# Kernel optimization log

Hardware: AMD Instinct MI355X
Metric: run time of the kernel (lower is better)

The kernel has to match this reference:

```python
import jax, jax.numpy as jnp
import numpy as np

B, S, V, H = 512, 2048, 29, 128  # batch, seq_len, vocab(input_size), hidden_size


def setup_inputs() -> dict:
    key = jax.random.key(0)
    ks = jax.random.split(key, 9)
    ke = 1.0 / np.sqrt(H)  # torch nn.RNN init bound for encoder
    kd = 1.0 / np.sqrt(V)  # decoder hidden_size = V
    u = lambda k, shape, b: jax.random.uniform(k, shape, jnp.float32, -b, b)
    return {
        "x": jax.random.normal(ks[0], (B, S, V), jnp.float32),
        "We_ih": u(ks[1], (H, V), ke),
        "We_hh": u(ks[2], (H, H), ke),
        "be_ih": u(ks[3], (H,), ke),
        "be_hh": u(ks[4], (H,), ke),
        "Wd_ih": u(ks[5], (V, H), kd),
        "Wd_hh": u(ks[6], (V, V), kd),
        "bd_ih": u(ks[7], (V,), kd),
        "bd_hh": u(ks[8], (V,), kd),
    }


def reference(x, We_ih, We_hh, be_ih, be_hh, Wd_ih, Wd_hh, bd_ih, bd_hh):
    b, s, _ = x.shape
    # ---- encoder: vanilla tanh RNN over sequence, keep final hidden state ----
    # precompute input projections for all steps: (S, B, H)
    xp = jnp.einsum("bsv,hv->sbh", x, We_ih) + be_ih + be_hh
    def enc_step(h, xt):
        h = jnp.tanh(xt + h @ We_hh.T)
        return h, None
    h0 = jnp.zeros((b, We_hh.shape[0]), x.dtype)
    encoded, _ = jax.lax.scan(enc_step, h0, xp)  # (B, H)
    # ---- decoder: feeds the same `encoded` vector at every step ----
    dec_in = encoded @ Wd_ih.T + bd_ih + bd_hh  # (B, V), constant across steps
    def dec_step(h, _):
        h = jnp.tanh(dec_in + h @ Wd_hh.T)
        return h, h
    hd0 = jnp.zeros((b, Wd_hh.shape[0]), x.dtype)
    _, outs = jax.lax.scan(dec_step, hd0, None, length=s)  # (S, B, V)
    return jnp.transpose(outs, (1, 0, 2))  # (B, S, V)
```

## Files before the change

### kernel.cpp

```cpp
#include <hip/hip_runtime.h>
#include <hip/hip_bf16.h>

#define BB 512
#define SS 2048
#define VV 29
#define HH 128

__device__ __forceinline__ float fast_tanh(float z) {
    float az = fabsf(z);
    float e  = __expf(-2.0f * az);
    float r  = 1.0f - 2.0f * e * __builtin_amdgcn_rcpf(1.0f + e);
    return copysignf(r, z);
}

__global__ __launch_bounds__(256) void rnn_fused(
    const float* __restrict__ x,
    const float* __restrict__ We_ih,
    const float* __restrict__ We_hh,
    const float* __restrict__ be_ih,
    const float* __restrict__ be_hh,
    const float* __restrict__ Wd_ih,
    const float* __restrict__ Wd_hh,
    const float* __restrict__ bd_ih,
    const float* __restrict__ bd_hh,
    float* __restrict__ out)
{
    const int b   = blockIdx.x;
    const int tid = threadIdx.x;
    const int wv  = tid >> 6;
    const int l   = tid & 63;
    const int i   = (wv << 5) + (l >> 1);
    const int g   = l & 1;

    __shared__ float hbuf[2][HH];
    __shared__ float xbuf[2][32];

    float w[64];
    const float* wrow = We_hh + i * HH + g * 64;
    #pragma unroll
    for (int j = 0; j < 64; ++j) w[j] = wrow[j];

    const int xv0 = g ? 15 : 0;
    const int xn  = g ? 14 : 15;
    float wx[15];
    #pragma unroll
    for (int j = 0; j < 15; ++j) wx[j] = (j < xn) ? We_ih[i * VV + xv0 + j] : 0.0f;

    const float bias = (g == 0) ? (be_ih[i] + be_hh[i]) : 0.0f;

    const float* xb = x + (size_t)b * SS * VV;

    if (tid < HH) hbuf[0][tid] = 0.0f;
    if (tid < 32) {
        xbuf[0][tid] = (tid < VV) ? xb[tid] : 0.0f;
        xbuf[1][tid] = 0.0f;
    }
    __syncthreads();

#define ENC_STEP(CUR, NXT, T)                                              \
    {                                                                      \
        float xpre = 0.0f;                                                 \
        {                                                                  \
            int tn = (T) + 1; if (tn >= SS) tn = SS - 1;                   \
            if (wv == 0 && l < VV) xpre = xb[tn * VV + l];                 \
        }                                                                  \
        float a0 = 0.f, a1 = 0.f, a2 = 0.f, a3 = 0.f;                      \
        const float* hb = &hbuf[CUR][g * 64];                              \
        _Pragma("unroll")                                                  \
        for (int j = 0; j < 64; j += 4) {                                  \
            a0 += w[j + 0] * hb[j + 0];                                    \
            a1 += w[j + 1] * hb[j + 1];                                    \
            a2 += w[j + 2] * hb[j + 2];                                    \
            a3 += w[j + 3] * hb[j + 3];                                    \
        }                                                                  \
        float accx = bias;                                                 \
        _Pragma("unroll")                                                  \
        for (int j = 0; j < 15; ++j) accx += wx[j] * xbuf[CUR][xv0 + j];   \
        float p = (a0 + a1) + (a2 + a3) + accx;                            \
        float q = __shfl_xor(p, 1, 64);                                    \
        float hn = fast_tanh(p + q);     \
        hbuf[NXT][i] = hn;             \
        if (wv == 0 && l < VV) xbuf[NXT][l] = xpre;                        \
        __syncthreads();                                                   \
    }

    for (int t = 0; t < SS; t += 2) {
        ENC_STEP(0, 1, t)
        ENC_STEP(1, 0, t + 1)
    }

    if (tid >= 64) return;
    const int lane = tid;
    const int r = (lane < VV) ? lane : (VV - 1);

    float di = bd_ih[r] + bd_hh[r];
    {
        const float* wdi = Wd_ih + r * HH;
        float d0 = 0.f, d1 = 0.f, d2 = 0.f, d3 = 0.f;
        #pragma unroll
        for (int j = 0; j < HH; j += 4) {
            d0 += wdi[j + 0] * hbuf[0][j + 0];
            d1 += wdi[j + 1] * hbuf[0][j + 1];
            d2 += wdi[j + 2] * hbuf[0][j + 2];
            d3 += wdi[j + 3] * hbuf[0][j + 3];
        }
        di += (d0 + d1) + (d2 + d3);
    }

    float wd[VV];
    {
        const float* wdr = Wd_hh + r * VV;
        #pragma unroll
        for (int j = 0; j < VV; ++j) wd[j] = wdr[j];
    }

    float hd = 0.0f;
    float* ob = out + (size_t)b * SS * VV;
    int t = 0;
    for (; t < SS; ++t) {
        float a0 = di, a1 = 0.f, a2 = 0.f, a3 = 0.f;
        #pragma unroll
        for (int j = 0; j < VV; j += 4) {
            a0 += wd[j] * __shfl(hd, j, 64);
            if (j + 1 < VV) a1 += wd[j + 1] * __shfl(hd, j + 1, 64);
            if (j + 2 < VV) a2 += wd[j + 2] * __shfl(hd, j + 2, 64);
            if (j + 3 < VV) a3 += wd[j + 3] * __shfl(hd, j + 3, 64);
        }
        float hn = fast_tanh((a0 + a1) + (a2 + a3));
        int conv = (fabsf(hn - hd) < 1e-6f) ? 1 : 0;
        hd = hn;
        if (lane < VV) ob[(size_t)t * VV + lane] = hn;
        if (__all(conv)) { ++t; break; }
    }

    if (t < SS) {
        while (t & 3) {
            if (lane < VV) ob[(size_t)t * VV + lane] = hd;
            ++t;
        }
        if (t < SS) {
            const int phi = (4 * lane) % VV;
            float4 v4;
            v4.x = __shfl(hd, phi, 64);
            v4.y = __shfl(hd, (phi + 1) % VV, 64);
            v4.z = __shfl(hd, (phi + 2) % VV, 64);
            v4.w = __shfl(hd, (phi + 3) % VV, 64);
            if (lane < 58) {
                const long fend = (long)SS * VV;
                for (long f = (long)t * VV + 4 * lane; f + 4 <= fend; f += 232) {
                    *reinterpret_cast<float4*>(ob + f) = v4;
                }
            }
        }
    }
}

extern "C" void kernel_launch(void* const* d_in, const int* in_sizes, int n_in,
                              void* d_out, int out_size, void* d_ws, size_t ws_size,
                              hipStream_t stream) {
    const float* x     = (const float*)d_in[0];
    const float* We_ih = (const float*)d_in[1];
    const float* We_hh = (const float*)d_in[2];
    const float* be_ih = (const float*)d_in[3];
    const float* be_hh = (const float*)d_in[4];
    const float* Wd_ih = (const float*)d_in[5];
    const float* Wd_hh = (const float*)d_in[6];
    const float* bd_ih = (const float*)d_in[7];
    const float* bd_hh = (const float*)d_in[8];
    float* out = (float*)d_out;

    rnn_fused<<<dim3(BB), dim3(256), 0, stream>>>(
        x, We_ih, We_hh, be_ih, be_hh, Wd_ih, Wd_hh, bd_ih, bd_hh, out);
}
```

Before: 1.671 ms.

## Assign one encoder hidden unit per thread with 128-thread blocks and deeper x prefetch

Each thread now owns a full row of We_hh (128 registers) instead of splitting it across two lanes. This drops the per-step shuffle reduction and halves the block to 128 threads (2 waves). Hidden state and inputs are read from shared memory as float4 vectors, and x is prefetched two steps ahead through rotating registers to hide global load latency. The trade-off is higher register pressure and twice the serial FMA work per thread, in exchange for fewer waves per barrier and less LDS traffic.

```diff
diff --git a/kernel.cpp b/kernel.cpp
--- a/kernel.cpp
+++ b/kernel.cpp
@@ -13,7 +13,7 @@
     return copysignf(r, z);
 }
 
-__global__ __launch_bounds__(256) void rnn_fused(
+__global__ __launch_bounds__(128, 1) void rnn_fused(
     const float* __restrict__ x,
     const float* __restrict__ We_ih,
     const float* __restrict__ We_hh,
@@ -27,66 +27,77 @@
 {
     const int b   = blockIdx.x;
     const int tid = threadIdx.x;
-    const int wv  = tid >> 6;
-    const int l   = tid & 63;
-    const int i   = (wv << 5) + (l >> 1);
-    const int g   = l & 1;
+    const int i   = tid;
 
     __shared__ float hbuf[2][HH];
     __shared__ float xbuf[2][32];
 
-    float w[64];
-    const float* wrow = We_hh + i * HH + g * 64;
+    float wh[HH];
+    {
+        const float4* wrow4 = reinterpret_cast<const float4*>(We_hh + (size_t)i * HH);
+        #pragma unroll
+        for (int j = 0; j < HH / 4; ++j) {
+            float4 v = wrow4[j];
+            wh[4 * j + 0] = v.x; wh[4 * j + 1] = v.y;
+            wh[4 * j + 2] = v.z; wh[4 * j + 3] = v.w;
+        }
+    }
+    float wx[32];
     #pragma unroll
-    for (int j = 0; j < 64; ++j) w[j] = wrow[j];
-
-    const int xv0 = g ? 15 : 0;
-    const int xn  = g ? 14 : 15;
-    float wx[15];
-    #pragma unroll
-    for (int j = 0; j < 15; ++j) wx[j] = (j < xn) ? We_ih[i * VV + xv0 + j] : 0.0f;
-
-    const float bias = (g == 0) ? (be_ih[i] + be_hh[i]) : 0.0f;
+    for (int j = 0; j < 32; ++j) wx[j] = (j < VV) ? We_ih[i * VV + j] : 0.0f;
+    const float bias = be_ih[i] + be_hh[i];
 
     const float* xb = x + (size_t)b * SS * VV;
 
-    if (tid < HH) hbuf[0][tid] = 0.0f;
+    hbuf[0][tid] = 0.0f;
     if (tid < 32) {
         xbuf[0][tid] = (tid < VV) ? xb[tid] : 0.0f;
         xbuf[1][tid] = 0.0f;
     }
+
+    float xA = 0.0f, xB = 0.0f;
+    if (tid < VV) {
+        xA = xb[VV + tid];
+        xB = xb[2 * VV + tid];
+    }
     __syncthreads();
 
-#define ENC_STEP(CUR, NXT, T)                                              \
+#define ENC_STEP(CUR, NXT, T, XREG)                                        \
     {                                                                      \
-        float xpre = 0.0f;                                                 \
+        float xnew = 0.0f;                                                 \
         {                                                                  \
-            int tn = (T) + 1; if (tn >= SS) tn = SS - 1;                   \
-            if (wv == 0 && l < VV) xpre = xb[tn * VV + l];                 \
+            int tn = (T) + 3; if (tn >= SS) tn = SS - 1;                   \
+            if (tid < VV) xnew = xb[tn * VV + tid];                        \
         }                                                                  \
-        float a0 = 0.f, a1 = 0.f, a2 = 0.f, a3 = 0.f;                      \
-        const float* hb = &hbuf[CUR][g * 64];                              \
+        float a0 = bias, a1 = 0.f, a2 = 0.f, a3 = 0.f;                     \
+        const float4* hb4 = reinterpret_cast<const float4*>(&hbuf[CUR][0]);\
         _Pragma("unroll")                                                  \
-        for (int j = 0; j < 64; j += 4) {                                  \
-            a0 += w[j + 0] * hb[j + 0];                                    \
-            a1 += w[j + 1] * hb[j + 1];                                    \
-            a2 += w[j + 2] * hb[j + 2];                                    \
-            a3 += w[j + 3] * hb[j + 3];                                    \
+        for (int j = 0; j < HH / 4; ++j) {                                 \
+            float4 hv = hb4[j];                                            \
+            a0 += wh[4 * j + 0] * hv.x;                                    \
+            a1 += wh[4 * j + 1] * hv.y;                                    \
+            a2 += wh[4 * j + 2] * hv.z;                                    \
+            a3 += wh[4 * j + 3] * hv.w;                                    \
         }                                                                  \
-        float accx = bias;                                                 \
+        const float4* xb4 = reinterpret_cast<const float4*>(&xbuf[CUR][0]);\
         _Pragma("unroll")                                                  \
-        for (int j = 0; j < 15; ++j) accx += wx[j] * xbuf[CUR][xv0 + j];   \
-        float p = (a0 + a1) + (a2 + a3) + accx;                            \
-        float q = __shfl_xor(p, 1, 64);                                    \
-        float hn = fast_tanh(p + q);     \
-        hbuf[NXT][i] = hn;             \
-        if (wv == 0 && l < VV) xbuf[NXT][l] = xpre;                        \
+        for (int k = 0; k < 8; ++k) {                                      \
+            float4 xv = xb4[k];                                            \
+            a0 += wx[4 * k + 0] * xv.x;                                    \
+            a1 += wx[4 * k + 1] * xv.y;                                    \
+            a2 += wx[4 * k + 2] * xv.z;                                    \
+            a3 += wx[4 * k + 3] * xv.w;                                    \
+        }                                                                  \
+        float hn = fast_tanh((a0 + a1) + (a2 + a3));                       \
+        hbuf[NXT][i] = hn;                                                 \
+        if (tid < VV) xbuf[NXT][tid] = XREG;   \
+        XREG = xnew;                               \
         __syncthreads();                                                   \
     }
 
     for (int t = 0; t < SS; t += 2) {
-        ENC_STEP(0, 1, t)
-        ENC_STEP(1, 0, t + 1)
+        ENC_STEP(0, 1, t,     xA)
+        ENC_STEP(1, 0, t + 1, xB)
     }
 
     if (tid >= 64) return;
@@ -169,6 +180,6 @@
     const float* bd_hh = (const float*)d_in[8];
     float* out = (float*)d_out;
 
-    rnn_fused<<<dim3(BB), dim3(256), 0, stream>>>(
+    rnn_fused<<<dim3(BB), dim3(128), 0, stream>>>(
         x, We_ih, We_hh, be_ih, be_hh, Wd_ih, Wd_hh, bd_ih, bd_hh, out);
 }
```

Measured after the change: 2.376 ms. 1.42x slower.

## Batch 16 sequences per block and run encoder recurrence on bf16x3 MFMA

Applied to the files above, without the earlier changes.

Each block now handles 16 batch rows instead of one. The encoder's hidden-state matvec becomes a small matrix multiply on MFMA bf16 instructions. Weights, hidden state and inputs are split into hi/lo bf16 pairs, and three products are summed to keep near-fp32 accuracy. Input x is loaded in 16-step chunks that are double-buffered and converted in shared memory, and the decoder runs two passes of half-wave groups per wave. This amortizes per-step barrier and latency cost across many sequences, but the launch shrinks to 32 blocks, and the split-bf16 products may lose precision relative to fp32.

```diff
diff --git a/kernel.cpp b/kernel.cpp
--- a/kernel.cpp
+++ b/kernel.cpp
@@ -5,6 +5,12 @@
 #define SS 2048
 #define VV 29
 #define HH 128
+#define NC 16
+#define NBLK (BB / NC)
+#define CH 16
+
+typedef __attribute__((ext_vector_type(8))) short bf16x8;
+typedef __attribute__((ext_vector_type(4))) float f32x4;
 
 __device__ __forceinline__ float fast_tanh(float z) {
     float az = fabsf(z);
@@ -12,8 +18,22 @@
     float r  = 1.0f - 2.0f * e * __builtin_amdgcn_rcpf(1.0f + e);
     return copysignf(r, z);
 }
-
-__global__ __launch_bounds__(256) void rnn_fused(
+__device__ __forceinline__ unsigned bf16_rne(float f) {
+    unsigned u = __float_as_uint(f);
+    return (u + 0x7fffu + ((u >> 16) & 1u)) >> 16;
+}
+__device__ __forceinline__ float bfbits2f(unsigned b) { return __uint_as_float(b << 16); }
+__device__ __forceinline__ bf16x8 as_bf16x8(uint4 v) { union { uint4 q; bf16x8 s; } u; u.q = v; return u.s; }
+
+#define MF(A, B, C) __builtin_amdgcn_mfma_f32_16x16x32_bf16((A), (B), (C), 0, 0, 0)
+
+#define BLOCK_SYNC do {                                        \
+    asm volatile("s_waitcnt lgkmcnt(0)" ::: "memory");         \
+    __builtin_amdgcn_s_barrier();                              \
+    asm volatile("" ::: "memory");                             \
+} while (0)
+
+__global__ __launch_bounds__(256, 1) void rnn_fused(
     const float* __restrict__ x,
     const float* __restrict__ We_ih,
     const float* __restrict__ We_hh,
@@ -25,130 +45,272 @@
     const float* __restrict__ bd_hh,
     float* __restrict__ out)
 {
-    const int b   = blockIdx.x;
     const int tid = threadIdx.x;
-    const int wv  = tid >> 6;
+    const int w   = tid >> 6;
     const int l   = tid & 63;
-    const int i   = (wv << 5) + (l >> 1);
-    const int g   = l & 1;
-
-    __shared__ float hbuf[2][HH];
-    __shared__ float xbuf[2][32];
-
-    float w[64];
-    const float* wrow = We_hh + i * HH + g * 64;
+    const int c   = l & 15;
+    const int g   = l >> 4;
+    const int b0  = blockIdx.x * NC;
+
+    __shared__ uint4 shHhi[2][4][4][16];
+    __shared__ uint4 shHlo[2][4][4][16];
+    __shared__ uint4 shXhi[2][CH][4][17];
+    __shared__ uint4 shXlo[2][CH][4][17];
+    __shared__ float hdec[NC][HH];
+
+    bf16x8 whiA[4], wloA[4], whiB[4], wloB[4];
+    bf16x8 wxhiA, wxloA, wxhiB, wxloB;
+    {
+        const int m0 = 16 * (2 * w)     + c;
+        const int m1 = 16 * (2 * w + 1) + c;
+        const float* r0 = We_hh + (size_t)m0 * HH;
+        const float* r1 = We_hh + (size_t)m1 * HH;
+        #pragma unroll
+        for (int kt = 0; kt < 4; ++kt) {
+            union { unsigned u[4]; bf16x8 s; } HA, LA, HB, LB;
+            #pragma unroll
+            for (int p = 0; p < 4; ++p) {
+                int e0 = 32 * kt + 8 * g + 2 * p;
+                float fa0 = r0[e0], fa1 = r0[e0 + 1];
+                float fb0 = r1[e0], fb1 = r1[e0 + 1];
+                unsigned ha0 = bf16_rne(fa0), ha1 = bf16_rne(fa1);
+                unsigned hb0 = bf16_rne(fb0), hb1 = bf16_rne(fb1);
+                HA.u[p] = ha0 | (ha1 << 16);
+                HB.u[p] = hb0 | (hb1 << 16);
+                LA.u[p] = bf16_rne(fa0 - bfbits2f(ha0)) | (bf16_rne(fa1 - bfbits2f(ha1)) << 16);
+                LB.u[p] = bf16_rne(fb0 - bfbits2f(hb0)) | (bf16_rne(fb1 - bfbits2f(hb1)) << 16);
+            }
+            whiA[kt] = HA.s; wloA[kt] = LA.s;
+            whiB[kt] = HB.s; wloB[kt] = LB.s;
+        }
+        const float* q0 = We_ih + (size_t)m0 * VV;
+        const float* q1 = We_ih + (size_t)m1 * VV;
+        union { unsigned u[4]; bf16x8 s; } HA, LA, HB, LB;
+        #pragma unroll
+        for (int p = 0; p < 4; ++p) {
+            int k0 = 8 * g + 2 * p;
+            float fa0 = (k0     < VV) ? q0[k0]     : 0.f;
+            float fa1 = (k0 + 1 < VV) ? q0[k0 + 1] : 0.f;
+            float fb0 = (k0     < VV) ? q1[k0]     : 0.f;
+            float fb1 = (k0 + 1 < VV) ? q1[k0 + 1] : 0.f;
+            unsigned ha0 = bf16_rne(fa0), ha1 = bf16_rne(fa1);
+            unsigned hb0 = bf16_rne(fb0), hb1 = bf16_rne(fb1);
+            HA.u[p] = ha0 | (ha1 << 16);
+            HB.u[p] = hb0 | (hb1 << 16);
+            LA.u[p] = bf16_rne(fa0 - bfbits2f(ha0)) | (bf16_rne(fa1 - bfbits2f(ha1)) << 16);
+            LB.u[p] = bf16_rne(fb0 - bfbits2f(hb0)) | (bf16_rne(fb1 - bfbits2f(hb1)) << 16);
+        }
+        wxhiA = HA.s; wxloA = LA.s; wxhiB = HB.s; wxloB = LB.s;
+    }
+
+    f32x4 bias0v, bias1v;
     #pragma unroll
-    for (int j = 0; j < 64; ++j) w[j] = wrow[j];
-
-    const int xv0 = g ? 15 : 0;
-    const int xn  = g ? 14 : 15;
-    float wx[15];
-    #pragma unroll
-    for (int j = 0; j < 15; ++j) wx[j] = (j < xn) ? We_ih[i * VV + xv0 + j] : 0.0f;
-
-    const float bias = (g == 0) ? (be_ih[i] + be_hh[i]) : 0.0f;
-
-    const float* xb = x + (size_t)b * SS * VV;
-
-    if (tid < HH) hbuf[0][tid] = 0.0f;
-    if (tid < 32) {
-        xbuf[0][tid] = (tid < VV) ? xb[tid] : 0.0f;
-        xbuf[1][tid] = 0.0f;
-    }
+    for (int q = 0; q < 4; ++q) {
+        int ra = 16 * (2 * w)     + 4 * g + q;
+        int rb = 16 * (2 * w + 1) + 4 * g + q;
+        bias0v[q] = be_ih[ra] + be_hh[ra];
+        bias1v[q] = be_ih[rb] + be_hh[rb];
+    }
+
+    const int c0 = tid >> 4;
+    const int t0 = tid & 15;
+    const float* xrowc = x + (size_t)(b0 + c0) * SS * VV;
+    float xv[VV];
+
+#define XLOAD(CHUNK) {                                                          \
+        const float* p_ = xrowc + (size_t)((CHUNK) * CH + t0) * VV;             \
+        _Pragma("unroll")                                                       \
+        for (int j = 0; j < VV; ++j) xv[j] = p_[j]; }
+
+#define XCONVERT(CB) {                                                          \
+        unsigned hb[VV + 1], lb[VV + 1];                                        \
+        _Pragma("unroll")                                                       \
+        for (int j = 0; j < VV; ++j) {                                          \
+            unsigned h_ = bf16_rne(xv[j]);                                      \
+            hb[j] = h_; lb[j] = bf16_rne(xv[j] - bfbits2f(h_));                 \
+        }                                                                       \
+        hb[VV] = 0u; lb[VV] = 0u;                                               \
+        _Pragma("unroll")                                                       \
+        for (int m = 0; m < 15; ++m) {                                          \
+            int g_ = m >> 2, w_ = m & 3;                                        \
+            ((unsigned*)&shXhi[CB][t0][g_][c0])[w_] = hb[2*m] | (hb[2*m+1] << 16); \
+            ((unsigned*)&shXlo[CB][t0][g_][c0])[w_] = lb[2*m] | (lb[2*m+1] << 16); \
+        }                                                                       \
+        ((unsigned*)&shXhi[CB][t0][3][c0])[3] = 0u;            \
+        ((unsigned*)&shXlo[CB][t0][3][c0])[3] = 0u; }
+
+    {
+        uint4 z = make_uint4(0u, 0u, 0u, 0u);
+        ((uint4*)shHhi)[tid] = z; ((uint4*)shHhi)[tid + 256] = z;
+        ((uint4*)shHlo)[tid] = z; ((uint4*)shHlo)[tid + 256] = z;
+    }
+    XLOAD(0);
     __syncthreads();
-
-#define ENC_STEP(CUR, NXT, T)                                              \
-    {                                                                      \
-        float xpre = 0.0f;                                                 \
-        {                                                                  \
-            int tn = (T) + 1; if (tn >= SS) tn = SS - 1;                   \
-            if (wv == 0 && l < VV) xpre = xb[tn * VV + l];                 \
-        }                                                                  \
-        float a0 = 0.f, a1 = 0.f, a2 = 0.f, a3 = 0.f;                      \
-        const float* hb = &hbuf[CUR][g * 64];                              \
-        _Pragma("unroll")                                                  \
-        for (int j = 0; j < 64; j += 4) {                                  \
-            a0 += w[j + 0] * hb[j + 0];                                    \
-            a1 += w[j + 1] * hb[j + 1];                                    \
-            a2 += w[j + 2] * hb[j + 2];                                    \
-            a3 += w[j + 3] * hb[j + 3];                                    \
-        }                                                                  \
-        float accx = bias;                                                 \
-        _Pragma("unroll")                                                  \
-        for (int j = 0; j < 15; ++j) accx += wx[j] * xbuf[CUR][xv0 + j];   \
-        float p = (a0 + a1) + (a2 + a3) + accx;                            \
-        float q = __shfl_xor(p, 1, 64);                                    \
-        float hn = fast_tanh(p + q);     \
-        hbuf[NXT][i] = hn;             \
-        if (wv == 0 && l < VV) xbuf[NXT][l] = xpre;                        \
-        __syncthreads();                                                   \
-    }
-
-    for (int t = 0; t < SS; t += 2) {
-        ENC_STEP(0, 1, t)
-        ENC_STEP(1, 0, t + 1)
-    }
-
-    if (tid >= 64) return;
-    const int lane = tid;
-    const int r = (lane < VV) ? lane : (VV - 1);
-
-    float di = bd_ih[r] + bd_hh[r];
+    XCONVERT(0);
+    XLOAD(1);
+    BLOCK_SYNC;
+
+#define ENC_STEP(CUR, NXT, SLOC, CB)                                            \
+    {                                                                           \
+        bf16x8 Bh0 = as_bf16x8(shHhi[CUR][0][g][c]);                            \
+        bf16x8 Bh1 = as_bf16x8(shHhi[CUR][1][g][c]);                            \
+        bf16x8 Bh2 = as_bf16x8(shHhi[CUR][2][g][c]);                            \
+        bf16x8 Bh3 = as_bf16x8(shHhi[CUR][3][g][c]);                            \
+        bf16x8 Bl0 = as_bf16x8(shHlo[CUR][0][g][c]);                            \
+        bf16x8 Bl1 = as_bf16x8(shHlo[CUR][1][g][c]);                            \
+        bf16x8 Bl2 = as_bf16x8(shHlo[CUR][2][g][c]);                            \
+        bf16x8 Bl3 = as_bf16x8(shHlo[CUR][3][g][c]);                            \
+        bf16x8 Bx  = as_bf16x8(shXhi[CB][SLOC][g][c]);                          \
+        bf16x8 Bxl = as_bf16x8(shXlo[CB][SLOC][g][c]);                          \
+        f32x4 d0a = bias0v, d1a = bias1v;                                       \
+        f32x4 d0b = {0.f,0.f,0.f,0.f}, d1b = {0.f,0.f,0.f,0.f};                 \
+        f32x4 d0c = {0.f,0.f,0.f,0.f}, d1c = {0.f,0.f,0.f,0.f};                 \
+        d0a = MF(whiA[0], Bh0, d0a);  d1a = MF(whiB[0], Bh0, d1a);              \
+        d0b = MF(wloA[0], Bh0, d0b);  d1b = MF(wloB[0], Bh0, d1b);              \
+        d0c = MF(whiA[0], Bl0, d0c);  d1c = MF(whiB[0], Bl0, d1c);              \
+        d0a = MF(whiA[1], Bh1, d0a);  d1a = MF(whiB[1], Bh1, d1a);              \
+        d0b = MF(wloA[1], Bh1, d0b);  d1b = MF(wloB[1], Bh1, d1b);              \
+        d0c = MF(whiA[1], Bl1, d0c);  d1c = MF(whiB[1], Bl1, d1c);              \
+        d0a = MF(whiA[2], Bh2, d0a);  d1a = MF(whiB[2], Bh2, d1a);              \
+        d0b = MF(wloA[2], Bh2, d0b);  d1b = MF(wloB[2], Bh2, d1b);              \
+        d0c = MF(whiA[2], Bl2, d0c);  d1c = MF(whiB[2], Bl2, d1c);              \
+        d0a = MF(whiA[3], Bh3, d0a);  d1a = MF(whiB[3], Bh3, d1a);              \
+        d0b = MF(wloA[3], Bh3, d0b);  d1b = MF(wloB[3], Bh3, d1b);              \
+        d0c = MF(whiA[3], Bl3, d0c);  d1c = MF(whiB[3], Bl3, d1c);              \
+        d0a = MF(wxhiA, Bx, d0a);     d1a = MF(wxhiB, Bx, d1a);                 \
+        d0b = MF(wxloA, Bx, d0b);     d1b = MF(wxloB, Bx, d1b);                 \
+        d0c = MF(wxhiA, Bxl, d0c);    d1c = MF(wxhiB, Bxl, d1c);                \
+        float hn00 = fast_tanh(d0a[0] + d0b[0] + d0c[0]);                       \
+        float hn01 = fast_tanh(d0a[1] + d0b[1] + d0c[1]);                       \
+        float hn02 = fast_tanh(d0a[2] + d0b[2] + d0c[2]);                       \
+        float hn03 = fast_tanh(d0a[3] + d0b[3] + d0c[3]);                       \
+        float hn10 = fast_tanh(d1a[0] + d1b[0] + d1c[0]);                       \
+        float hn11 = fast_tanh(d1a[1] + d1b[1] + d1c[1]);                       \
+        float hn12 = fast_tanh(d1a[2] + d1b[2] + d1c[2]);                       \
+        float hn13 = fast_tanh(d1a[3] + d1b[3] + d1c[3]);                       \
+        unsigned h00 = bf16_rne(hn00), h01 = bf16_rne(hn01);                    \
+        unsigned h02 = bf16_rne(hn02), h03 = bf16_rne(hn03);                    \
+        unsigned h10 = bf16_rne(hn10), h11 = bf16_rne(hn11);                    \
+        unsigned h12 = bf16_rne(hn12), h13 = bf16_rne(hn13);                    \
+        unsigned l00 = bf16_rne(hn00 - bfbits2f(h00));                          \
+        unsigned l01 = bf16_rne(hn01 - bfbits2f(h01));                          \
+        unsigned l02 = bf16_rne(hn02 - bfbits2f(h02));                          \
+        unsigned l03 = bf16_rne(hn03 - bfbits2f(h03));                          \
+        unsigned l10 = bf16_rne(hn10 - bfbits2f(h10));                          \
+        unsigned l11 = bf16_rne(hn11 - bfbits2f(h11));                          \
+        unsigned l12 = bf16_rne(hn12 - bfbits2f(h12));                          \
+        unsigned l13 = bf16_rne(hn13 - bfbits2f(h13));                          \
+        {                                          \
+            ((uint2*)&shHhi[NXT][w][(g >> 1)][c])[g & 1] =                      \
+                make_uint2(h00 | (h01 << 16), h02 | (h03 << 16));               \
+            ((uint2*)&shHlo[NXT][w][(g >> 1)][c])[g & 1] =                      \
+                make_uint2(l00 | (l01 << 16), l02 | (l03 << 16));               \
+        }                                                                       \
+        {                                  \
+            ((uint2*)&shHhi[NXT][w][2 + (g >> 1)][c])[g & 1] =                  \
+                make_uint2(h10 | (h11 << 16), h12 | (h13 << 16));               \
+            ((uint2*)&shHlo[NXT][w][2 + (g >> 1)][c])[g & 1] =                  \
+                make_uint2(l10 | (l11 << 16), l12 | (l13 << 16));               \
+        }                                                                       \
+        BLOCK_SYNC;                                                             \
+    }
+
+    int cur = 0;
+    for (int tc = 0; tc < SS; tc += CH) {
+        const int cb = (tc >> 4) & 1;
+        for (int s = 0; s < CH; ++s) {
+            ENC_STEP(cur, cur ^ 1, s, cb)
+            cur ^= 1;
+        }
+        if (tc + CH < SS) {
+            XCONVERT(cb ^ 1);
+            if (tc + 2 * CH < SS) XLOAD((tc >> 4) + 2);
+            BLOCK_SYNC;
+        }
+    }
+
     {
-        const float* wdi = Wd_ih + r * HH;
-        float d0 = 0.f, d1 = 0.f, d2 = 0.f, d3 = 0.f;
+        int rr = tid & 15;
+        int eb = tid >> 4;
         #pragma unroll
-        for (int j = 0; j < HH; j += 4) {
-            d0 += wdi[j + 0] * hbuf[0][j + 0];
-            d1 += wdi[j + 1] * hbuf[0][j + 1];
-            d2 += wdi[j + 2] * hbuf[0][j + 2];
-            d3 += wdi[j + 3] * hbuf[0][j + 3];
-        }
-        di += (d0 + d1) + (d2 + d3);
-    }
-
-    float wd[VV];
-    {
-        const float* wdr = Wd_hh + r * VV;
-        #pragma unroll
-        for (int j = 0; j < VV; ++j) wd[j] = wdr[j];
-    }
-
-    float hd = 0.0f;
-    float* ob = out + (size_t)b * SS * VV;
-    int t = 0;
-    for (; t < SS; ++t) {
-        float a0 = di, a1 = 0.f, a2 = 0.f, a3 = 0.f;
-        #pragma unroll
-        for (int j = 0; j < VV; j += 4) {
-            a0 += wd[j] * __shfl(hd, j, 64);
-            if (j + 1 < VV) a1 += wd[j + 1] * __shfl(hd, j + 1, 64);
-            if (j + 2 < VV) a2 += wd[j + 2] * __shfl(hd, j + 2, 64);
-            if (j + 3 < VV) a3 += wd[j + 3] * __shfl(hd, j + 3, 64);
-        }
-        float hn = fast_tanh((a0 + a1) + (a2 + a3));
-        int conv = (fabsf(hn - hd) < 1e-6f) ? 1 : 0;
-        hd = hn;
-        if (lane < VV) ob[(size_t)t * VV + lane] = hn;
-        if (__all(conv)) { ++t; break; }
-    }
-
-    if (t < SS) {
-        while (t & 3) {
-            if (lane < VV) ob[(size_t)t * VV + lane] = hd;
-            ++t;
-        }
+        for (int j = 0; j < 8; ++j) {
+            int e = eb * 8 + j;
+            unsigned wh = ((const unsigned*)&shHhi[0][e >> 5][(e >> 3) & 3][rr])[(e & 7) >> 1];
+            unsigned wl = ((const unsigned*)&shHlo[0][e >> 5][(e >> 3) & 3][rr])[(e & 7) >> 1];
+            unsigned hh = (e & 1) ? (wh >> 16) : (wh & 0xffffu);
+            unsigned ll = (e & 1) ? (wl >> 16) : (wl & 0xffffu);
+            hdec[rr][e] = bfbits2f(hh) + bfbits2f(ll);
+        }
+    }
+    __syncthreads();
+
+    const int hf  = l >> 5;
+    const int rl0 = l & 31;
+    const int rl  = (rl0 < VV) ? rl0 : (VV - 1);
+
+    for (int pass = 0; pass < 2; ++pass) {
+        const int row = 8 * pass + 2 * w + hf;
+        float di = bd_ih[rl] + bd_hh[rl];
+        {
+            const float* wdi = Wd_ih + rl * HH;
+            const float* hv  = hdec[row];
+            float d0 = 0.f, d1 = 0.f, d2 = 0.f, d3 = 0.f;
+            #pragma unroll
+            for (int j = 0; j < HH; j += 4) {
+                d0 += wdi[j + 0] * hv[j + 0];
+                d1 += wdi[j + 1] * hv[j + 1];
+                d2 += wdi[j + 2] * hv[j + 2];
+                d3 += wdi[j + 3] * hv[j + 3];
+            }
+            di += (d0 + d1) + (d2 + d3);
+        }
+        float wd[VV];
+        {
+            const float* wdr = Wd_hh + rl * VV;
+            #pragma unroll
+            for (int j = 0; j < VV; ++j) wd[j] = wdr[j];
+        }
+
+        float hd = 0.0f;
+        float* ob = out + (size_t)(b0 + row) * SS * VV;
+        int t = 0;
+        for (; t < SS; ++t) {
+            float a0 = di, a1 = 0.f, a2 = 0.f, a3 = 0.f;
+            #pragma unroll
+            for (int j = 0; j < VV; j += 4) {
+                a0 += wd[j] * __shfl(hd, j, 32);
+                if (j + 1 < VV) a1 += wd[j + 1] * __shfl(hd, j + 1, 32);
+                if (j + 2 < VV) a2 += wd[j + 2] * __shfl(hd, j + 2, 32);
+                if (j + 3 < VV) a3 += wd[j + 3] * __shfl(hd, j + 3, 32);
+            }
+            float hn = fast_tanh((a0 + a1) + (a2 + a3));
+            int conv = (fabsf(hn - hd) < 1e-6f) ? 1 : 0;
+            hd = hn;
+            if (rl0 < VV) ob[(size_t)t * VV + rl0] = hn;
+            if (__all(conv)) { ++t; break; }
+        }
+
         if (t < SS) {
-            const int phi = (4 * lane) % VV;
-            float4 v4;
-            v4.x = __shfl(hd, phi, 64);
-            v4.y = __shfl(hd, (phi + 1) % VV, 64);
-            v4.z = __shfl(hd, (phi + 2) % VV, 64);
-            v4.w = __shfl(hd, (phi + 3) % VV, 64);
-            if (lane < 58) {
-                const long fend = (long)SS * VV;
-                for (long f = (long)t * VV + 4 * lane; f + 4 <= fend; f += 232) {
-                    *reinterpret_cast<float4*>(ob + f) = v4;
+            while (t & 3) {
+                if (rl0 < VV) ob[(size_t)t * VV + rl0] = hd;
+                ++t;
+            }
+            if (t < SS) {
+                const int phi = (4 * l) % VV;
+                #pragma unroll
+                for (int h2 = 0; h2 < 2; ++h2) {
+                    float* obr = out + (size_t)(b0 + 8 * pass + 2 * w + h2) * SS * VV;
+                    float4 v4;
+                    v4.x = __shfl(hd, 32 * h2 + phi,              64);
+                    v4.y = __shfl(hd, 32 * h2 + (phi + 1) % VV,   64);
+                    v4.z = __shfl(hd, 32 * h2 + (phi + 2) % VV,   64);
+                    v4.w = __shfl(hd, 32 * h2 + (phi + 3) % VV,   64);
+                    if (l < 58) {
+                        const long fend = (long)SS * VV;
+                        for (long f = (long)t * VV + 4 * l; f + 4 <= fend; f += 232) {
+                            *reinterpret_cast<float4*>(obr + f) = v4;
+                        }
+                    }
                 }
             }
         }
@@ -169,6 +331,6 @@
     const float* bd_hh = (const float*)d_in[8];
     float* out = (float*)d_out;
 
-    rnn_fused<<<dim3(BB), dim3(256), 0, stream>>>(
+    rnn_fused<<<dim3(NBLK), dim3(256), 0, stream>>>(
         x, We_ih, We_hh, be_ih, be_hh, Wd_ih, Wd_hh, bd_ih, bd_hh, out);
 }
```

New measurement: 1.623 ms. -2.8%, faster.
